# Performance work log

Measured on AMD Instinct MI355X. Metric: run time of the kernel, lower is better.

The kernel has to match this reference:

```python
import jax, jax.numpy as jnp
import numpy as np
import math

D = 768
H = 8
DK = D // H
FF = 1024
EPS = 1e-5


def _layer_norm(x, g, b):
    m = jnp.mean(x, axis=-1, keepdims=True)
    v = jnp.mean((x - m) ** 2, axis=-1, keepdims=True)
    return (x - m) * jax.lax.rsqrt(v + EPS) * g + b


def _mha(x, attention_mask, Wq, bq, Wv, bv, g, b):
    # x: (B,S,D); attention_mask: (B,S,1) bool (True = masked/padding query row)
    B, S, _ = x.shape
    q = (x @ Wq + bq).reshape(B, S, H, DK).transpose(0, 2, 1, 3)  # (B,H,S,dk)
    # NOTE: original code uses the V projection for BOTH k and v (k = self.V(x))
    kv = (x @ Wv + bv).reshape(B, S, H, DK).transpose(0, 2, 1, 3)
    k = kv
    v = kv
    w = jnp.einsum('bhqd,bhkd->bhqk', q, k) / math.sqrt(DK)  # (B,H,S,S)
    pad = attention_mask[:, None, :, :]                      # (B,1,S,1) -> bcast (B,1,S,S)
    causal = jnp.triu(jnp.ones((S, S), dtype=bool), k=1)     # look-ahead mask
    mask = pad | causal
    w = jnp.where(mask, jnp.float32(-1e9), w)
    # NOTE: original uses nn.Softmax(dim=2) -> softmax over the QUERY axis
    score = jax.nn.softmax(w, axis=2)
    o = jnp.einsum('bhqk,bhkd->bhqd', score, v)              # (B,H,S,dk)
    o = o.transpose(0, 2, 1, 3).reshape(B, S, D)
    return _layer_norm(o + x, g, b)


def _ffn(x, W1, b1, W2, b2, g, b):
    h = jax.nn.relu(x @ W1 + b1)
    return _layer_norm(h @ W2 + b2 + x, g, b)


def setup_inputs() -> dict:
    key = jax.random.key(0)
    ks = jax.random.split(key, 16)
    B, S = 8, 1024
    sc = 0.02
    inp = {
        'x': jax.random.normal(ks[0], (B, S, D), dtype=jnp.float32),
        'attention_mask': jax.random.randint(ks[1], (B, S, 1), 0, 2).astype(bool),
    }
    for i, pre in enumerate(['a1', 'a2']):
        inp[pre + '_Wq'] = jax.random.normal(ks[2 + 4 * i], (D, D), dtype=jnp.float32) * sc
        inp[pre + '_bq'] = jnp.zeros((D,), dtype=jnp.float32)
        inp[pre + '_Wv'] = jax.random.normal(ks[3 + 4 * i], (D, D), dtype=jnp.float32) * sc
        inp[pre + '_bv'] = jnp.zeros((D,), dtype=jnp.float32)
        inp[pre + '_g'] = jnp.ones((D,), dtype=jnp.float32)
        inp[pre + '_b'] = jnp.zeros((D,), dtype=jnp.float32)
    inp['f_W1'] = jax.random.normal(ks[10], (D, FF), dtype=jnp.float32) * sc
    inp['f_b1'] = jnp.zeros((FF,), dtype=jnp.float32)
    inp['f_W2'] = jax.random.normal(ks[11], (FF, D), dtype=jnp.float32) * sc
    inp['f_b2'] = jnp.zeros((D,), dtype=jnp.float32)
    inp['f_g'] = jnp.ones((D,), dtype=jnp.float32)
    inp['f_b'] = jnp.zeros((D,), dtype=jnp.float32)
    return inp


def reference(x, attention_mask,
              a1_Wq, a1_bq, a1_Wv, a1_bv, a1_g, a1_b,
              a2_Wq, a2_bq, a2_Wv, a2_bv, a2_g, a2_b,
              f_W1, f_b1, f_W2, f_b2, f_g, f_b):
    x = _mha(x, attention_mask, a1_Wq, a1_bq, a1_Wv, a1_bv, a1_g, a1_b)
    x = _mha(x, attention_mask, a2_Wq, a2_bq, a2_Wv, a2_bv, a2_g, a2_b)
    x = _ffn(x, f_W1, f_b1, f_W2, f_b2, f_g, f_b)
    return x
```

## Files before the change

kernel.cpp:

```cpp
#include <hip/hip_runtime.h>
#include <cstddef>

#define BB 8
#define SS 1024
#define DD 768
#define HH 8
#define DKK 96
#define FFF 1024
#define MM (BB*SS)
#define QVW 1536
#define SM_SCALE 0.10206207261596577f
#define NTILES 16
#define NPAIR  136

typedef unsigned short ushort_t;
typedef short short8 __attribute__((ext_vector_type(8)));
typedef float f32x4 __attribute__((ext_vector_type(4)));
typedef ushort_t us4 __attribute__((ext_vector_type(4)));

__device__ __forceinline__ ushort_t f2b(float f) {
    union { float f; unsigned u; } x; x.f = f;
    unsigned r = x.u + 0x7fffu + ((x.u >> 16) & 1u);
    return (ushort_t)(r >> 16);
}
__device__ __forceinline__ float b2f(ushort_t u) {
    union { unsigned u; float f; } x; x.u = ((unsigned)u) << 16;
    return x.f;
}
__device__ __forceinline__ void gload16(const ushort_t* g, void* lds_base) {
    __builtin_amdgcn_global_load_lds(
        (const __attribute__((address_space(1))) unsigned int*)g,
        (__attribute__((address_space(3))) unsigned int*)lds_base, 16, 0, 0);
}

__global__ __launch_bounds__(256) void castWT(
    const float* __restrict__ W, ushort_t* __restrict__ Wt, int K, int N)
{
    __shared__ float T[32][33];
    const int tx = threadIdx.x & 31, ty = threadIdx.x >> 5;
    const int n0 = blockIdx.x * 32, k0 = blockIdx.y * 32;
    #pragma unroll
    for (int r = 0; r < 4; ++r)
        T[ty + 8*r][tx] = W[(size_t)(k0 + ty + 8*r) * N + n0 + tx];
    __syncthreads();
    #pragma unroll
    for (int r = 0; r < 4; ++r)
        Wt[(size_t)(n0 + ty + 8*r) * K + k0 + tx] = f2b(T[tx][ty + 8*r]);
}

__global__ __launch_bounds__(256) void castWT4(
    const float* __restrict__ Wa, const float* __restrict__ Wb,
    const float* __restrict__ Wc, const float* __restrict__ Wd,
    ushort_t* __restrict__ Ta, ushort_t* __restrict__ Tb,
    ushort_t* __restrict__ Tc, ushort_t* __restrict__ Td)
{
    __shared__ float T[32][33];
    const float* W; ushort_t* Wt;
    switch (blockIdx.z) {
        case 0:  W = Wa; Wt = Ta; break;
        case 1:  W = Wb; Wt = Tb; break;
        case 2:  W = Wc; Wt = Tc; break;
        default: W = Wd; Wt = Td; break;
    }
    const int tx = threadIdx.x & 31, ty = threadIdx.x >> 5;
    const int n0 = blockIdx.x * 32, k0 = blockIdx.y * 32;
    #pragma unroll
    for (int r = 0; r < 4; ++r)
        T[ty + 8*r][tx] = W[(size_t)(k0 + ty + 8*r) * DD + n0 + tx];
    __syncthreads();
    #pragma unroll
    for (int r = 0; r < 4; ++r)
        Wt[(size_t)(n0 + ty + 8*r) * DD + k0 + tx] = f2b(T[tx][ty + 8*r]);
}

__global__ __launch_bounds__(256) void cast_f2b(
    const float* __restrict__ in, ushort_t* __restrict__ out, int n4)
{
    const int i = blockIdx.x * 256 + threadIdx.x;
    if (i >= n4) return;
    const float4 v = ((const float4*)in)[i];
    us4 o; o.x = f2b(v.x); o.y = f2b(v.y); o.z = f2b(v.z); o.w = f2b(v.w);
    ((us4*)out)[i] = o;
}

template<int RELU>
__global__ __launch_bounds__(256) void gemm_bt(
    const ushort_t* __restrict__ A, const ushort_t* __restrict__ Bt,
    const float* __restrict__ bias, const float* __restrict__ bias2, int bN,
    ushort_t* __restrict__ C, int K, int N)
{
    __shared__ ushort_t S[128*136];
    ushort_t* As = S;
    ushort_t* Bs = S + 128*64;
    const int tid  = threadIdx.x;
    const int lane = tid & 63, wave = tid >> 6;
    const int wm = wave >> 1, wn = wave & 1;
    const int n = lane & 15, quad = lane >> 4;
    const int sx = n & 7;
    const int bm = blockIdx.y * 128, bn = blockIdx.x * 128;

    f32x4 acc[4][4];
    #pragma unroll
    for (int i = 0; i < 4; ++i)
        #pragma unroll
        for (int j = 0; j < 4; ++j) acc[i][j] = (f32x4){0.f, 0.f, 0.f, 0.f};

    for (int k0 = 0; k0 < K; k0 += 64) {
        #pragma unroll
        for (int it = 0; it < 4; ++it) {
            const int u   = (it*4 + wave)*64 + lane;
            const int row = u >> 3;
            const int c   = (u & 7) ^ (row & 7);
            gload16(A  + (size_t)(bm + row) * K + k0 + c*8, (char*)As + (it*4 + wave)*1024);
            gload16(Bt + (size_t)(bn + row) * K + k0 + c*8, (char*)Bs + (it*4 + wave)*1024);
        }
        __syncthreads();
        #pragma unroll
        for (int ks = 0; ks < 2; ++ks) {
            short8 af[4], bf[4];
            #pragma unroll
            for (int i = 0; i < 4; ++i)
                af[i] = *(short8*)&As[((wm*64 + i*16 + n)*8 + ((ks*4 + quad) ^ sx))*8];
            #pragma unroll
            for (int j = 0; j < 4; ++j)
                bf[j] = *(short8*)&Bs[((wn*64 + j*16 + n)*8 + ((ks*4 + quad) ^ sx))*8];
            #pragma unroll
            for (int i = 0; i < 4; ++i)
                #pragma unroll
                for (int j = 0; j < 4; ++j)
                    acc[i][j] = __builtin_amdgcn_mfma_f32_16x16x32_bf16(af[i], bf[j], acc[i][j], 0, 0, 0);
        }
        __syncthreads();
    }
    #pragma unroll
    for (int j = 0; j < 4; ++j) {
        const int col = wn*64 + j*16 + n;
        const int gcol = bn + col;
        const float bsv = (gcol < bN) ? bias[gcol] : bias2[gcol - bN];
        #pragma unroll
        for (int i = 0; i < 4; ++i) {
            const int lrow = wm*64 + i*16 + quad*4;
            #pragma unroll
            for (int r = 0; r < 4; ++r) {
                float v = acc[i][j][r] + bsv;
                if (RELU) v = fmaxf(v, 0.f);
                S[(lrow + r)*136 + col] = f2b(v);
            }
        }
    }
    __syncthreads();
    #pragma unroll
    for (int it = 0; it < 8; ++it) {
        const int u = it*256 + tid;
        const int grow = u >> 4, gc = u & 15;
        *(short8*)(C + (size_t)(bm + grow)*N + bn + gc*8) = *(short8*)&S[grow*136 + gc*8];
    }
}

__global__ __launch_bounds__(256) void attn_scores(
    const ushort_t* __restrict__ QV, const int* __restrict__ amask,
    ushort_t* __restrict__ E, float* __restrict__ lpart)
{
    __shared__ ushort_t Qs[64*128];
    __shared__ ushort_t Ks[64*128];
    __shared__ ushort_t Etile[64*72];
    __shared__ float colsum[4][64];
    __shared__ float padf[64];
    const int tid = threadIdx.x, lane = tid & 63, wave = tid >> 6;
    const int n = lane & 15, quad = lane >> 4;
    const int sx = n & 7;
    const int t = blockIdx.x;
    int qt = (int)((-1.f + sqrtf(1.f + 8.f*(float)t)) * 0.5f);
    if ((qt+1)*(qt+2)/2 <= t) ++qt;
    if (qt*(qt+1)/2 > t) --qt;
    const int kt = t - qt*(qt+1)/2;
    const int q0 = qt*64, k0 = kt*64;
    const int h = blockIdx.y, b = blockIdx.z;
    const ushort_t* Qh = QV + (size_t)b*SS*QVW + h*DKK;
    const ushort_t* Kh = QV + (size_t)b*SS*QVW + DD + h*DKK;

    #pragma unroll
    for (int it = 0; it < 4; ++it) {
        const int u = (it*4 + wave)*64 + lane;
        const int row = u >> 4;
        const int c = (u & 15) ^ (row & 7);
        if (c < 12) {
            gload16(Qh + (size_t)(q0 + row)*QVW + c*8, (char*)Qs + (it*4 + wave)*1024);
            gload16(Kh + (size_t)(k0 + row)*QVW + c*8, (char*)Ks + (it*4 + wave)*1024);
        }
    }
    if (tid < 64) padf[tid] = (amask[b*SS + q0 + tid] != 0) ? 1.f : 0.f;
    __syncthreads();

    ushort_t* Et = E + (size_t)(b*HH + h)*NPAIR*4096 + (size_t)(qt*(qt+1)/2 + kt)*4096;

    #pragma unroll
    for (int ns = 0; ns < 4; ++ns) {
        f32x4 sa = (f32x4){0.f, 0.f, 0.f, 0.f};
        #pragma unroll
        for (int ks = 0; ks < 3; ++ks) {
            const short8 aq = *(short8*)&Qs[((wave*16 + n)*16 + ((ks*4 + quad) ^ sx))*8];
            const short8 bk = *(short8*)&Ks[((ns*16   + n)*16 + ((ks*4 + quad) ^ sx))*8];
            sa = __builtin_amdgcn_mfma_f32_16x16x32_bf16(aq, bk, sa, 0, 0, 0);
        }
        const int kl = ns*16 + n;
        const int keyg = k0 + kl;
        float s = 0.f;
        #pragma unroll
        for (int r = 0; r < 4; ++r) {
            const int qrow = wave*16 + quad*4 + r;
            const bool dead = (padf[qrow] != 0.f) || (keyg > q0 + qrow);
            const float e = dead ? 0.f : __expf(sa[r] * SM_SCALE);
            s += e;
            Etile[qrow*72 + kl] = f2b(e);
        }
        s += __shfl_xor(s, 16);
        s += __shfl_xor(s, 32);
        if (quad == 0) colsum[wave][kl] = s;
    }
    __syncthreads();
    #pragma unroll
    for (int it = 0; it < 2; ++it) {
        const int u = it*256 + tid;
        const int grow = u >> 3, gc = u & 7;
        *(short8*)(Et + grow*64 + gc*8) = *(short8*)&Etile[grow*72 + gc*8];
    }
    if (tid < 64) {
        const float s = colsum[0][tid] + colsum[1][tid] + colsum[2][tid] + colsum[3][tid];
        lpart[((size_t)(b*HH + h)*NTILES + qt)*SS + k0 + tid] = s;
    }
}

__global__ __launch_bounds__(256) void transpose_scale(
    const ushort_t* __restrict__ QV, const float* __restrict__ lpart,
    ushort_t* __restrict__ Vt)
{
    __shared__ ushort_t T[64][104];
    __shared__ float rlv[64];
    const int tid = threadIdx.x;
    const int k0 = blockIdx.x * 64, h = blockIdx.y, b = blockIdx.z;
    const ushort_t* src = QV + (size_t)b*SS*QVW + DD + h*DKK;
    for (int s = tid; s < 768; s += 256) {
        const int r = s / 12, c = s % 12;
        *(short8*)&T[r][c*8] = *(const short8*)(src + (size_t)(k0 + r)*QVW + c*8);
    }
    if (tid < 64) {
        const float* lp = lpart + (size_t)(b*HH + h)*NTILES*SS;
        float l = 0.f;
        for (int qt = k0 >> 6; qt < NTILES; ++qt) l += lp[(size_t)qt*SS + k0 + tid];
        rlv[tid] = (l > 0.f) ? (1.f / l) : 0.f;
    }
    __syncthreads();
    ushort_t* dst = Vt + ((size_t)b*HH + h)*DKK*SS;
    for (int s = tid; s < 768; s += 256) {
        const int dk = s >> 3, c = s & 7;
        short8 v;
        #pragma unroll
        for (int i = 0; i < 8; ++i)
            v[i] = (short)f2b(b2f(T[c*8 + i][dk]) * rlv[c*8 + i]);
        *(short8*)(dst + (size_t)dk*SS + k0 + c*8) = v;
    }
}

__global__ __launch_bounds__(256) void attn_pv(
    const ushort_t* __restrict__ E, const ushort_t* __restrict__ Vt,
    ushort_t* __restrict__ O)
{
    __shared__ ushort_t Es[64*64];
    __shared__ ushort_t Vs[96*64];
    const int tid = threadIdx.x, lane = tid & 63, wave = tid >> 6;
    const int n = lane & 15, quad = lane >> 4;
    const int sx = n & 7;
    const int px = blockIdx.x;
    const int h = blockIdx.y, b = blockIdx.z;
    const ushort_t* Eb  = E + (size_t)(b*HH + h)*NPAIR*4096;
    const ushort_t* Vth = Vt + ((size_t)b*HH + h)*DKK*SS;

    #pragma unroll
    for (int half = 0; half < 2; ++half) {
        const int qt = half ? (15 - px) : px;
        const int q0 = qt * 64;
        f32x4 acc[6];
        #pragma unroll
        for (int t = 0; t < 6; ++t) acc[t] = (f32x4){0.f, 0.f, 0.f, 0.f};
        const ushort_t* Eq = Eb + (size_t)(qt*(qt+1)/2)*4096;

        for (int kt = 0; kt <= qt; ++kt) {
            const ushort_t* Et = Eq + (size_t)kt*4096;
            #pragma unroll
            for (int it = 0; it < 2; ++it) {
                const int u = (it*4 + wave)*64 + lane;
                const int row = u >> 3, c = (u & 7) ^ (row & 7);
                gload16(Et + (size_t)row*64 + c*8, (char*)Es + (it*4 + wave)*1024);
            }
            #pragma unroll
            for (int it = 0; it < 3; ++it) {
                const int u = (it*4 + wave)*64 + lane;
                const int row = u >> 3, c = (u & 7) ^ (row & 7);
                gload16(Vth + (size_t)row*SS + kt*64 + c*8, (char*)Vs + (it*4 + wave)*1024);
            }
            __syncthreads();
            #pragma unroll
            for (int kk = 0; kk < 2; ++kk) {
                const short8 ae = *(short8*)&Es[((wave*16 + n)*8 + ((kk*4 + quad) ^ sx))*8];
                #pragma unroll
                for (int nt = 0; nt < 6; ++nt) {
                    const short8 bv = *(short8*)&Vs[((nt*16 + n)*8 + ((kk*4 + quad) ^ sx))*8];
                    acc[nt] = __builtin_amdgcn_mfma_f32_16x16x32_bf16(ae, bv, acc[nt], 0, 0, 0);
                }
            }
            __syncthreads();
        }
        #pragma unroll
        for (int nt = 0; nt < 6; ++nt) {
            #pragma unroll
            for (int r = 0; r < 4; ++r) {
                const int q = q0 + wave*16 + quad*4 + r;
                O[((size_t)b*SS + q)*DD + h*DKK + nt*16 + n] = f2b(acc[nt][r]);
            }
        }
    }
}

__device__ __forceinline__ float block_sum256(float s, float* tmp4)
{
    #pragma unroll
    for (int off = 32; off > 0; off >>= 1) s += __shfl_down(s, off);
    __syncthreads();
    if ((threadIdx.x & 63) == 0) tmp4[threadIdx.x >> 6] = s;
    __syncthreads();
    return tmp4[0] + tmp4[1] + tmp4[2] + tmp4[3];
}

template<int XBF, int RBF, int OUTF32>
__global__ __launch_bounds__(256) void resid_ln(
    const void* __restrict__ X, const void* __restrict__ R,
    const float* __restrict__ g, const float* __restrict__ beta,
    ushort_t* __restrict__ OutB, float* __restrict__ OutF)
{
    __shared__ float tmp4[4];
    const int row = blockIdx.x;
    const int tid = threadIdx.x;
    float v[3], s = 0.f;
    #pragma unroll
    for (int i = 0; i < 3; ++i) {
        const size_t idx = (size_t)row * DD + tid + 256*i;
        const float xv = XBF ? b2f(((const ushort_t*)X)[idx]) : ((const float*)X)[idx];
        const float rv = RBF ? b2f(((const ushort_t*)R)[idx]) : ((const float*)R)[idx];
        v[i] = xv + rv;
        s += v[i];
    }
    const float mu = block_sum256(s, tmp4) * (1.f / DD);
    float qv = 0.f;
    #pragma unroll
    for (int i = 0; i < 3; ++i) { const float d = v[i] - mu; qv += d * d; }
    const float inv = rsqrtf(block_sum256(qv, tmp4) * (1.f / DD) + 1e-5f);
    #pragma unroll
    for (int i = 0; i < 3; ++i) {
        const int c = tid + 256*i;
        const float o = (v[i] - mu) * inv * g[c] + beta[c];
        if (OUTF32) OutF[(size_t)row * DD + c] = o;
        else        OutB[(size_t)row * DD + c] = f2b(o);
    }
}

extern "C" void kernel_launch(void* const* d_in, const int* in_sizes, int n_in,
                              void* d_out, int out_size, void* d_ws, size_t ws_size,
                              hipStream_t stream)
{
    (void)in_sizes; (void)n_in; (void)out_size; (void)ws_size;
    const float* x0    = (const float*)d_in[0];
    const int*   amask = (const int*)d_in[1];
    const float* a1_Wq = (const float*)d_in[2];
    const float* a1_bq = (const float*)d_in[3];
    const float* a1_Wv = (const float*)d_in[4];
    const float* a1_bv = (const float*)d_in[5];
    const float* a1_g  = (const float*)d_in[6];
    const float* a1_b  = (const float*)d_in[7];
    const float* a2_Wq = (const float*)d_in[8];
    const float* a2_bq = (const float*)d_in[9];
    const float* a2_Wv = (const float*)d_in[10];
    const float* a2_bv = (const float*)d_in[11];
    const float* a2_g  = (const float*)d_in[12];
    const float* a2_b  = (const float*)d_in[13];
    const float* f_W1  = (const float*)d_in[14];
    const float* f_b1  = (const float*)d_in[15];
    const float* f_W2  = (const float*)d_in[16];
    const float* f_b2  = (const float*)d_in[17];
    const float* f_g   = (const float*)d_in[18];
    const float* f_b   = (const float*)d_in[19];

    char* ws = (char*)d_ws;
    size_t off = 0;
    auto alloc = [&](size_t bytes) { void* p = ws + off; off += (bytes + 255) & ~(size_t)255; return p; };
    ushort_t* WqvT1 = (ushort_t*)alloc((size_t)QVW*DD*2);
    ushort_t* WqvT2 = (ushort_t*)alloc((size_t)QVW*DD*2);
    ushort_t* W1T   = (ushort_t*)alloc((size_t)DD*FFF*2);
    ushort_t* W2T   = (ushort_t*)alloc((size_t)DD*FFF*2);
    ushort_t* xb0   = (ushort_t*)alloc((size_t)MM*DD*2);
    ushort_t* xb1   = (ushort_t*)alloc((size_t)MM*DD*2);
    ushort_t* xb2   = (ushort_t*)alloc((size_t)MM*DD*2);
    ushort_t* Ob    = (ushort_t*)alloc((size_t)MM*DD*2);
    ushort_t* QVb   = (ushort_t*)alloc((size_t)MM*QVW*2);
    ushort_t* hb    = QVb;
    ushort_t* Vtb   = (ushort_t*)alloc((size_t)MM*DD*2);
    float* lpart = (float*)alloc((size_t)BB*HH*NTILES*SS*4);
    ushort_t* Ebuf = (ushort_t*)alloc((size_t)BB*HH*NPAIR*4096*2);
    float* out = (float*)d_out;

    const dim3 blk(256);
    const dim3 gsc(NPAIR, HH, BB);
    const dim3 gpv(NTILES/2, HH, BB);
    const dim3 gtr(SS/64, HH, BB);
    const dim3 gqv(QVW/128, MM/128);
    const dim3 gf1(FFF/128, MM/128);
    const dim3 gf2(DD/128, MM/128);

    castWT4<<<dim3(DD/32, DD/32, 4), blk, 0, stream>>>(
        a1_Wq, a1_Wv, a2_Wq, a2_Wv,
        WqvT1, WqvT1 + (size_t)DD*DD, WqvT2, WqvT2 + (size_t)DD*DD);
    castWT<<<dim3(FFF/32, DD/32), blk, 0, stream>>>(f_W1, W1T, DD, FFF);
    castWT<<<dim3(DD/32, FFF/32), blk, 0, stream>>>(f_W2, W2T, FFF, DD);
    cast_f2b<<<(MM*DD/4 + 255)/256, blk, 0, stream>>>(x0, xb0, MM*DD/4);

    gemm_bt<0><<<gqv, blk, 0, stream>>>(xb0, WqvT1, a1_bq, a1_bv, DD, QVb, DD, QVW);
    attn_scores<<<gsc, blk, 0, stream>>>(QVb, amask, Ebuf, lpart);
    transpose_scale<<<gtr, blk, 0, stream>>>(QVb, lpart, Vtb);
    attn_pv<<<gpv, blk, 0, stream>>>(Ebuf, Vtb, Ob);
    resid_ln<1,0,0><<<dim3(MM), blk, 0, stream>>>(Ob, x0, a1_g, a1_b, xb1, nullptr);

    gemm_bt<0><<<gqv, blk, 0, stream>>>(xb1, WqvT2, a2_bq, a2_bv, DD, QVb, DD, QVW);
    attn_scores<<<gsc, blk, 0, stream>>>(QVb, amask, Ebuf, lpart);
    transpose_scale<<<gtr, blk, 0, stream>>>(QVb, lpart, Vtb);
    attn_pv<<<gpv, blk, 0, stream>>>(Ebuf, Vtb, Ob);
    resid_ln<1,1,0><<<dim3(MM), blk, 0, stream>>>(Ob, xb1, a2_g, a2_b, xb2, nullptr);

    gemm_bt<1><<<gf1, blk, 0, stream>>>(xb2, W1T, f_b1, f_b1, FFF, hb, DD, FFF);
    gemm_bt<0><<<gf2, blk, 0, stream>>>(hb, W2T, f_b2, f_b2, DD, Ob, FFF, DD);
    resid_ln<1,1,1><<<dim3(MM), blk, 0, stream>>>(Ob, xb2, f_g, f_b, nullptr, out);
}
```

Before: 419.1 us.

## Recompute attention exponentials in PV kernel instead of materializing E buffer

The scores kernel now only computes column sums of exp(scores) and no longer writes the bf16 exponential matrix E to global memory. The PV kernel loads Q and K tiles, recomputes QK^T and the masked exponentials into shared memory per key tile, then multiplies by the prescaled V. This removes the large E write and read traffic (about 70 MB per attention layer) at the cost of doing the QK^T MFMAs and exps twice, and raises shared memory use in the PV kernel.

```diff
diff --git a/kernel.cpp b/kernel.cpp
--- a/kernel.cpp
+++ b/kernel.cpp
@@ -157,13 +157,12 @@
     }
 }
 
-__global__ __launch_bounds__(256) void attn_scores(
+__global__ __launch_bounds__(256) void attn_sums(
     const ushort_t* __restrict__ QV, const int* __restrict__ amask,
-    ushort_t* __restrict__ E, float* __restrict__ lpart)
+    float* __restrict__ lpart)
 {
     __shared__ ushort_t Qs[64*128];
     __shared__ ushort_t Ks[64*128];
-    __shared__ ushort_t Etile[64*72];
     __shared__ float colsum[4][64];
     __shared__ float padf[64];
     const int tid = threadIdx.x, lane = tid & 63, wave = tid >> 6;
@@ -192,8 +191,6 @@
     if (tid < 64) padf[tid] = (amask[b*SS + q0 + tid] != 0) ? 1.f : 0.f;
     __syncthreads();
 
-    ushort_t* Et = E + (size_t)(b*HH + h)*NPAIR*4096 + (size_t)(qt*(qt+1)/2 + kt)*4096;
-
     #pragma unroll
     for (int ns = 0; ns < 4; ++ns) {
         f32x4 sa = (f32x4){0.f, 0.f, 0.f, 0.f};
@@ -212,19 +209,12 @@
             const bool dead = (padf[qrow] != 0.f) || (keyg > q0 + qrow);
             const float e = dead ? 0.f : __expf(sa[r] * SM_SCALE);
             s += e;
-            Etile[qrow*72 + kl] = f2b(e);
         }
         s += __shfl_xor(s, 16);
         s += __shfl_xor(s, 32);
         if (quad == 0) colsum[wave][kl] = s;
     }
     __syncthreads();
-    #pragma unroll
-    for (int it = 0; it < 2; ++it) {
-        const int u = it*256 + tid;
-        const int grow = u >> 3, gc = u & 7;
-        *(short8*)(Et + grow*64 + gc*8) = *(short8*)&Etile[grow*72 + gc*8];
-    }
     if (tid < 64) {
         const float s = colsum[0][tid] + colsum[1][tid] + colsum[2][tid] + colsum[3][tid];
         lpart[((size_t)(b*HH + h)*NTILES + qt)*SS + k0 + tid] = s;
@@ -262,44 +252,84 @@
     }
 }
 
-__global__ __launch_bounds__(256) void attn_pv(
-    const ushort_t* __restrict__ E, const ushort_t* __restrict__ Vt,
-    ushort_t* __restrict__ O)
-{
+__global__ __launch_bounds__(256) void attn_pv_re(
+    const ushort_t* __restrict__ QV, const int* __restrict__ amask,
+    const ushort_t* __restrict__ Vt, ushort_t* __restrict__ O)
+{
+    __shared__ ushort_t Qs[64*128];
+    __shared__ ushort_t Ks[64*128];
+    __shared__ ushort_t Vs[96*64];
     __shared__ ushort_t Es[64*64];
-    __shared__ ushort_t Vs[96*64];
+    __shared__ float padf[64];
     const int tid = threadIdx.x, lane = tid & 63, wave = tid >> 6;
     const int n = lane & 15, quad = lane >> 4;
     const int sx = n & 7;
     const int px = blockIdx.x;
     const int h = blockIdx.y, b = blockIdx.z;
-    const ushort_t* Eb  = E + (size_t)(b*HH + h)*NPAIR*4096;
+    const ushort_t* Qh = QV + (size_t)b*SS*QVW + h*DKK;
+    const ushort_t* Kh = QV + (size_t)b*SS*QVW + DD + h*DKK;
     const ushort_t* Vth = Vt + ((size_t)b*HH + h)*DKK*SS;
 
     #pragma unroll
     for (int half = 0; half < 2; ++half) {
         const int qt = half ? (15 - px) : px;
         const int q0 = qt * 64;
+
+        #pragma unroll
+        for (int it = 0; it < 4; ++it) {
+            const int u = (it*4 + wave)*64 + lane;
+            const int row = u >> 4;
+            const int c = (u & 15) ^ (row & 7);
+            if (c < 12)
+                gload16(Qh + (size_t)(q0 + row)*QVW + c*8, (char*)Qs + (it*4 + wave)*1024);
+        }
+        if (tid < 64) padf[tid] = (amask[b*SS + q0 + tid] != 0) ? 1.f : 0.f;
+
         f32x4 acc[6];
         #pragma unroll
         for (int t = 0; t < 6; ++t) acc[t] = (f32x4){0.f, 0.f, 0.f, 0.f};
-        const ushort_t* Eq = Eb + (size_t)(qt*(qt+1)/2)*4096;
 
         for (int kt = 0; kt <= qt; ++kt) {
-            const ushort_t* Et = Eq + (size_t)kt*4096;
-            #pragma unroll
-            for (int it = 0; it < 2; ++it) {
+            const int k0 = kt * 64;
+            #pragma unroll
+            for (int it = 0; it < 4; ++it) {
                 const int u = (it*4 + wave)*64 + lane;
-                const int row = u >> 3, c = (u & 7) ^ (row & 7);
-                gload16(Et + (size_t)row*64 + c*8, (char*)Es + (it*4 + wave)*1024);
+                const int row = u >> 4;
+                const int c = (u & 15) ^ (row & 7);
+                if (c < 12)
+                    gload16(Kh + (size_t)(k0 + row)*QVW + c*8, (char*)Ks + (it*4 + wave)*1024);
             }
             #pragma unroll
             for (int it = 0; it < 3; ++it) {
                 const int u = (it*4 + wave)*64 + lane;
                 const int row = u >> 3, c = (u & 7) ^ (row & 7);
-                gload16(Vth + (size_t)row*SS + kt*64 + c*8, (char*)Vs + (it*4 + wave)*1024);
+                gload16(Vth + (size_t)row*SS + k0 + c*8, (char*)Vs + (it*4 + wave)*1024);
             }
             __syncthreads();
+
+            #pragma unroll
+            for (int ns = 0; ns < 4; ++ns) {
+                f32x4 sa = (f32x4){0.f, 0.f, 0.f, 0.f};
+                #pragma unroll
+                for (int ks = 0; ks < 3; ++ks) {
+                    const short8 aq = *(short8*)&Qs[((wave*16 + n)*16 + ((ks*4 + quad) ^ sx))*8];
+                    const short8 bk = *(short8*)&Ks[((ns*16   + n)*16 + ((ks*4 + quad) ^ sx))*8];
+                    sa = __builtin_amdgcn_mfma_f32_16x16x32_bf16(aq, bk, sa, 0, 0, 0);
+                }
+                const int kl = ns*16 + n;
+                const int keyg = k0 + kl;
+                #pragma unroll
+                for (int r = 0; r < 4; ++r) {
+                    const int lq = quad*4 + r;
+                    const int trow = wave*16 + lq;
+                    const bool dead = (padf[trow] != 0.f) || (keyg > q0 + trow);
+                    const float e = dead ? 0.f : __expf(sa[r] * SM_SCALE);
+                    Es[trow*64 + (((kl >> 3) ^ (lq & 7)) * 8) + (kl & 7)] = f2b(e);
+                }
+            }
+            asm volatile("s_waitcnt lgkmcnt(0)" ::: "memory");
+            __builtin_amdgcn_sched_barrier(0);
+
             #pragma unroll
             for (int kk = 0; kk < 2; ++kk) {
                 const short8 ae = *(short8*)&Es[((wave*16 + n)*8 + ((kk*4 + quad) ^ sx))*8];
@@ -405,7 +435,6 @@
     ushort_t* hb    = QVb;
     ushort_t* Vtb   = (ushort_t*)alloc((size_t)MM*DD*2);
     float* lpart = (float*)alloc((size_t)BB*HH*NTILES*SS*4);
-    ushort_t* Ebuf = (ushort_t*)alloc((size_t)BB*HH*NPAIR*4096*2);
     float* out = (float*)d_out;
 
     const dim3 blk(256);
@@ -424,15 +453,15 @@
     cast_f2b<<<(MM*DD/4 + 255)/256, blk, 0, stream>>>(x0, xb0, MM*DD/4);
 
     gemm_bt<0><<<gqv, blk, 0, stream>>>(xb0, WqvT1, a1_bq, a1_bv, DD, QVb, DD, QVW);
-    attn_scores<<<gsc, blk, 0, stream>>>(QVb, amask, Ebuf, lpart);
+    attn_sums<<<gsc, blk, 0, stream>>>(QVb, amask, lpart);
     transpose_scale<<<gtr, blk, 0, stream>>>(QVb, lpart, Vtb);
-    attn_pv<<<gpv, blk, 0, stream>>>(Ebuf, Vtb, Ob);
+    attn_pv_re<<<gpv, blk, 0, stream>>>(QVb, amask, Vtb, Ob);
     resid_ln<1,0,0><<<dim3(MM), blk, 0, stream>>>(Ob, x0, a1_g, a1_b, xb1, nullptr);
 
     gemm_bt<0><<<gqv, blk, 0, stream>>>(xb1, WqvT2, a2_bq, a2_bv, DD, QVb, DD, QVW);
-    attn_scores<<<gsc, blk, 0, stream>>>(QVb, amask, Ebuf, lpart);
+    attn_sums<<<gsc, blk, 0, stream>>>(QVb, amask, lpart);
     transpose_scale<<<gtr, blk, 0, stream>>>(QVb, lpart, Vtb);
-    attn_pv<<<gpv, blk, 0, stream>>>(Ebuf, Vtb, Ob);
+    attn_pv_re<<<gpv, blk, 0, stream>>>(QVb, amask, Vtb, Ob);
     resid_ln<1,1,0><<<dim3(MM), blk, 0, stream>>>(Ob, xb1, a2_g, a2_b, xb2, nullptr);
 
     gemm_bt<1><<<gf1, blk, 0, stream>>>(xb2, W1T, f_b1, f_b1, FFF, hb, DD, FFF);
```

Measured after the change: 433.1 us. +3.3%, slower.
